# Optimization experiments

Hardware: AMD Instinct MI355X
Metric: run time of the kernel (lower is better)

## Reference

```python
import jax, jax.numpy as jnp
import numpy as np

N_NODES = 100000
N_EDGES = 1_600_000
N_ROIS = 400
HIDDEN = 128
N_GRAPHS = 512
OUT = 2


def setup_inputs() -> dict:
    key = jax.random.key(0)
    ks = jax.random.split(key, 7)
    x = jax.random.normal(ks[0], (N_NODES, N_ROIS), dtype=jnp.float32)
    edge_index = jax.random.randint(ks[1], (2, N_EDGES), 0, N_NODES, dtype=jnp.int32)
    # sorted graph-assignment vector; prepend arange so every graph id is non-empty
    rnd = jax.random.randint(ks[2], (N_NODES - N_GRAPHS,), 0, N_GRAPHS, dtype=jnp.int32)
    batch = jnp.sort(jnp.concatenate([jnp.arange(N_GRAPHS, dtype=jnp.int32), rnd]))
    W = jax.random.normal(ks[3], (N_ROIS, HIDDEN), dtype=jnp.float32) / np.float32(np.sqrt(N_ROIS))
    b = jnp.zeros((HIDDEN,), dtype=jnp.float32)
    lin_W = jax.random.normal(ks[4], (HIDDEN, OUT), dtype=jnp.float32) / np.float32(np.sqrt(HIDDEN))
    lin_b = jnp.zeros((OUT,), dtype=jnp.float32)
    return {"x": x, "edge_index": edge_index, "batch": batch,
            "W": W, "b": b, "lin_W": lin_W, "lin_b": lin_b}


def reference(x, edge_index, batch, W, b, lin_W, lin_b):
    N = x.shape[0]
    # GCNConv: add self-loops, symmetric normalization D^-1/2 (A+I) D^-1/2
    loops = jnp.arange(N, dtype=edge_index.dtype)
    row = jnp.concatenate([edge_index[0], loops])  # source
    col = jnp.concatenate([edge_index[1], loops])  # target
    deg = jax.ops.segment_sum(jnp.ones_like(col, dtype=x.dtype), col, num_segments=N)
    dinv = jnp.where(deg > 0, jax.lax.rsqrt(deg), 0.0)
    norm = dinv[row] * dinv[col]                   # [E+N]
    h = x @ W                                      # [N, H] transform before propagate
    msg = h[row] * norm[:, None]                   # [E+N, H]
    agg = jax.ops.segment_sum(msg, col, num_segments=N) + b
    act = jax.nn.relu(agg)                         # [N, H]
    # global max pool over graph ids (all segments guaranteed non-empty)
    pooled = jax.ops.segment_max(act, batch, num_segments=N_GRAPHS)  # [G, H]
    logits = pooled @ lin_W + lin_b                # [G, OUT]
    return logits, pooled
```

## Files before the change

kernel.cpp:

```cpp
#include <hip/hip_runtime.h>
#include <hip/hip_bf16.h>

#define N_NODES 100000
#define N_EDGES 1600000
#define N_ROIS  400
#define RKP     416
#define HID     128
#define N_GRAPHS 512
#define NOUT    2
#define NBUCK   391
#define BCAP    8192
#define ECH     4096
#define NPW     16

typedef __attribute__((ext_vector_type(8))) short short8;
typedef __attribute__((ext_vector_type(4))) float f32x4;

static __device__ __forceinline__ unsigned short f2bf(float f) {
  unsigned u = __float_as_uint(f);
  u += 0x7fffu + ((u >> 16) & 1u);
  return (unsigned short)(u >> 16);
}
static __device__ __forceinline__ float bf2f(unsigned short h) {
  return __uint_as_float(((unsigned)h) << 16);
}

static __device__ __forceinline__ void gload_lds16(const unsigned short* g, short* l) {
  __builtin_amdgcn_global_load_lds(
      (const __attribute__((address_space(1))) void*)g,
      (__attribute__((address_space(3))) void*)l, 16, 0, 0);
}

__global__ __launch_bounds__(256) void bucket_k(
    const int* __restrict__ row, const int* __restrict__ col,
    int* __restrict__ bcnt, unsigned int* __restrict__ pairs) {
  __shared__ int hist[NBUCK];
  __shared__ int base[NBUCK];
  int t = threadIdx.x;
  for (int b = t; b < NBUCK; b += 256) hist[b] = 0;
  __syncthreads();
  int e0 = blockIdx.x * ECH;
  unsigned int pk[16];
  int bk[16], rk[16];
#pragma unroll
  for (int i = 0; i < 16; ++i) {
    int e = e0 + t + i * 256;
    if (e < N_EDGES) {
      int r = row[e], c = col[e];
      bk[i] = c >> 8;
      pk[i] = ((unsigned)r << 8) | (unsigned)(c & 255);
      rk[i] = atomicAdd(&hist[bk[i]], 1);
    } else bk[i] = -1;
  }
  __syncthreads();
  for (int b = t; b < NBUCK; b += 256)
    base[b] = (hist[b] > 0) ? atomicAdd(&bcnt[b], hist[b]) : 0;
  __syncthreads();
#pragma unroll
  for (int i = 0; i < 16; ++i)
    if (bk[i] >= 0) {
      int p = base[bk[i]] + rk[i];
      if (p < BCAP) pairs[(size_t)bk[i] * BCAP + p] = pk[i];
    }
}

__global__ __launch_bounds__(256) void csr_build_k(
    const unsigned int* __restrict__ pairs, const int* __restrict__ bcnt,
    int* __restrict__ csr_row, int* __restrict__ offs, int* __restrict__ cnt,
    float* __restrict__ dinv) {
  __shared__ unsigned int ep[BCAP];
  __shared__ int h[256];
  __shared__ int sc[256];
  __shared__ int cur[256];
  int b = blockIdx.x;
  int t = threadIdx.x;
  int m = min(bcnt[b], BCAP);
  size_t base = (size_t)b * BCAP;
  for (int j = t; j < m; j += 256) ep[j] = pairs[base + j];
  h[t] = 0;
  __syncthreads();
  for (int j = t; j < m; j += 256) atomicAdd(&h[ep[j] & 255u], 1);
  __syncthreads();
  int myc = h[t];
  int mycp = (myc + 3) & ~3;
  sc[t] = mycp;
  __syncthreads();
  for (int off = 1; off < 256; off <<= 1) {
    int v = (t >= off) ? sc[t - off] : 0;
    __syncthreads();
    sc[t] += v;
    __syncthreads();
  }
  int loff = sc[t] - mycp;
  cur[t] = loff;
  int node = b * 256 + t;
  if (node < N_NODES) {
    cnt[node] = myc;
    offs[node] = (int)base + loff;
    dinv[node] = rsqrtf((float)(myc + 1));
  }
  __syncthreads();
  for (int j = t; j < m; j += 256) {
    unsigned int e = ep[j];
    int pos = atomicAdd(&cur[e & 255u], 1);
    if (pos < BCAP) csr_row[base + pos] = (int)(e >> 8);
  }
}

__global__ void prep_wt_k(const float* __restrict__ W, unsigned short* __restrict__ Wf) {
  int idx = blockIdx.x * blockDim.x + threadIdx.x;
  if (idx >= 13 * 8 * 64 * 8) return;
  int u    = idx & 7;
  int lane = (idx >> 3) & 63;
  int nt   = (idx >> 9) & 7;
  int kk5  = idx >> 12;
  int n = nt * 16 + (lane & 15);
  int k = kk5 * 32 + (lane >> 4) * 8 + u;
  Wf[idx] = (k < N_ROIS) ? f2bf(W[k * HID + n]) : (unsigned short)0;
}

__global__ __launch_bounds__(512, 4) void gemm_k(
    const float* __restrict__ x, const unsigned short* __restrict__ Wf,
    const float* __restrict__ dinv, unsigned short* __restrict__ hp) {
  __shared__ __align__(16) short Bs[28672];
  int t = threadIdx.x;
  int lane = t & 63, wv = t >> 6;
  int mrow = lane & 15, kg = lane >> 4;
  int row0 = blockIdx.x * 128;
  int arow = row0 + wv * 16 + mrow;
  bool rowok = arow < N_NODES;
  const float* xp = x + (size_t)arow * N_ROIS;

  f32x4 acc[8];
#pragma unroll
  for (int i = 0; i < 8; ++i) acc[i] = (f32x4){0.f, 0.f, 0.f, 0.f};

#pragma unroll
  for (int c = 0; c < 7; ++c) {
    int ch = wv * 7 + c;
    gload_lds16(Wf + (size_t)ch * 512 + lane * 8, &Bs[ch * 512]);
  }
  asm volatile("s_waitcnt vmcnt(0)" ::: "memory");
  __syncthreads();

#pragma unroll
  for (int kf = 0; kf < 7; ++kf) {
    int k0 = kf * 32 + kg * 8;
    short8 a8;
    if (rowok && k0 + 8 <= N_ROIS) {
      float4 f0 = *(const float4*)(xp + k0);
      float4 f1 = *(const float4*)(xp + k0 + 4);
      a8[0] = (short)f2bf(f0.x); a8[1] = (short)f2bf(f0.y);
      a8[2] = (short)f2bf(f0.z); a8[3] = (short)f2bf(f0.w);
      a8[4] = (short)f2bf(f1.x); a8[5] = (short)f2bf(f1.y);
      a8[6] = (short)f2bf(f1.z); a8[7] = (short)f2bf(f1.w);
    } else {
#pragma unroll
      for (int u = 0; u < 8; ++u) {
        int k = k0 + u;
        float f = (rowok && k < N_ROIS) ? xp[k] : 0.f;
        a8[u] = (short)f2bf(f);
      }
    }
#pragma unroll
    for (int nt = 0; nt < 8; ++nt) {
      short8 bf = *(const short8*)&Bs[(kf * 8 + nt) * 512 + lane * 8];
      acc[nt] = __builtin_amdgcn_mfma_f32_16x16x32_bf16(a8, bf, acc[nt], 0, 0, 0);
    }
  }
  __syncthreads();

#pragma unroll
  for (int c = 0; c < 6; ++c) {
    int ch = wv * 6 + c;
    gload_lds16(Wf + (size_t)(56 + ch) * 512 + lane * 8, &Bs[ch * 512]);
  }
  asm volatile("s_waitcnt vmcnt(0)" ::: "memory");
  __syncthreads();

#pragma unroll
  for (int kf = 0; kf < 6; ++kf) {
    int k0 = (kf + 7) * 32 + kg * 8;
    short8 a8;
    if (rowok && k0 + 8 <= N_ROIS) {
      float4 f0 = *(const float4*)(xp + k0);
      float4 f1 = *(const float4*)(xp + k0 + 4);
      a8[0] = (short)f2bf(f0.x); a8[1] = (short)f2bf(f0.y);
      a8[2] = (short)f2bf(f0.z); a8[3] = (short)f2bf(f0.w);
      a8[4] = (short)f2bf(f1.x); a8[5] = (short)f2bf(f1.y);
      a8[6] = (short)f2bf(f1.z); a8[7] = (short)f2bf(f1.w);
    } else {
#pragma unroll
      for (int u = 0; u < 8; ++u) {
        int k = k0 + u;
        float f = (rowok && k < N_ROIS) ? xp[k] : 0.f;
        a8[u] = (short)f2bf(f);
      }
    }
#pragma unroll
    for (int nt = 0; nt < 8; ++nt) {
      short8 bf = *(const short8*)&Bs[(kf * 8 + nt) * 512 + lane * 8];
      acc[nt] = __builtin_amdgcn_mfma_f32_16x16x32_bf16(a8, bf, acc[nt], 0, 0, 0);
    }
  }

#pragma unroll
  for (int r = 0; r < 4; ++r) {
    int grow = row0 + wv * 16 + kg * 4 + r;
    if (grow < N_NODES) {
      float di = dinv[grow];
      unsigned short* op = hp + (size_t)grow * HID + mrow;
#pragma unroll
      for (int nt = 0; nt < 8; ++nt) op[nt * 16] = f2bf(di * acc[nt][r]);
    }
  }
}

static __device__ __forceinline__ void acc8(float* a, uint4 u) {
  a[0] += bf2f((unsigned short)(u.x));
  a[1] += bf2f((unsigned short)(u.x >> 16));
  a[2] += bf2f((unsigned short)(u.y));
  a[3] += bf2f((unsigned short)(u.y >> 16));
  a[4] += bf2f((unsigned short)(u.z));
  a[5] += bf2f((unsigned short)(u.z >> 16));
  a[6] += bf2f((unsigned short)(u.w));
  a[7] += bf2f((unsigned short)(u.w >> 16));
}

__global__ __launch_bounds__(256) void gather_k(
    const unsigned short* __restrict__ hp, const int* __restrict__ csr_row,
    const int* __restrict__ offs, const int* __restrict__ cnt,
    const float* __restrict__ dinv, const int* __restrict__ batch,
    const float* __restrict__ bias, unsigned int* __restrict__ pooled_bits) {
  int wave = (blockIdx.x * blockDim.x + threadIdx.x) >> 6;
  int lane = threadIdx.x & 63;
  int g  = lane >> 4;
  int cg = lane & 15;
  int n0 = wave * NPW;
  if (n0 >= N_NODES) return;
  int nend = min(n0 + NPW, N_NODES);
  float bv[8];
  {
    float4 b0 = *(const float4*)(bias + cg * 8);
    float4 b1 = *(const float4*)(bias + cg * 8 + 4);
    bv[0] = b0.x; bv[1] = b0.y; bv[2] = b0.z; bv[3] = b0.w;
    bv[4] = b1.x; bv[5] = b1.y; bv[6] = b1.z; bv[7] = b1.w;
  }
  float rm[8];
#pragma unroll
  for (int k = 0; k < 8; ++k) rm[k] = 0.f;
  int cur_g = batch[n0];

  for (int i = n0; i < nend; ++i) {
    int start = offs[i];
    int m = cnt[i];
    float a[8];
#pragma unroll
    for (int k = 0; k < 8; ++k) a[k] = 0.f;
    if (g == 0) {
      uint4 u = *(const uint4*)(hp + (size_t)i * HID + cg * 8);
      acc8(a, u);
    }
    for (int j = 0; j < m; j += 4) {
      int4 q = *(const int4*)(csr_row + start + j);
      int s = (g == 0) ? q.x : (g == 1) ? q.y : (g == 2) ? q.z : q.w;
      if (j + g < m) {
        uint4 u = *(const uint4*)(hp + (size_t)s * HID + cg * 8);
        acc8(a, u);
      }
    }
#pragma unroll
    for (int k = 0; k < 8; ++k) {
      a[k] += __shfl_xor(a[k], 16);
      a[k] += __shfl_xor(a[k], 32);
    }
    float di = dinv[i];
    int gb = batch[i];
    if (gb != cur_g) {
      if (lane < 16) {
#pragma unroll
        for (int k = 0; k < 8; ++k)
          atomicMax(&pooled_bits[cur_g * HID + cg * 8 + k], __float_as_uint(rm[k]));
      }
#pragma unroll
      for (int k = 0; k < 8; ++k) rm[k] = 0.f;
      cur_g = gb;
    }
#pragma unroll
    for (int k = 0; k < 8; ++k)
      rm[k] = fmaxf(rm[k], fmaxf(fmaf(di, a[k], bv[k]), 0.f));
  }
  if (lane < 16) {
#pragma unroll
    for (int k = 0; k < 8; ++k)
      atomicMax(&pooled_bits[cur_g * HID + cg * 8 + k], __float_as_uint(rm[k]));
  }
}

__global__ void logits_k(const float* __restrict__ pooled, const float* __restrict__ lin_W,
                         const float* __restrict__ lin_b, float* __restrict__ out) {
  int t = blockIdx.x * blockDim.x + threadIdx.x;
  if (t < N_GRAPHS * NOUT) {
    int g = t >> 1, o = t & 1;
    float s = lin_b[o];
    const float* pg = pooled + g * HID;
#pragma unroll 8
    for (int k = 0; k < HID; ++k) s = fmaf(pg[k], lin_W[k * NOUT + o], s);
    out[t] = s;
  }
}

extern "C" void kernel_launch(void* const* d_in, const int* in_sizes, int n_in,
                              void* d_out, int out_size, void* d_ws, size_t ws_size,
                              hipStream_t stream) {
  (void)in_sizes; (void)n_in; (void)ws_size;
  const float* x     = (const float*)d_in[0];
  const int*   ei    = (const int*)d_in[1];
  const int*   row   = ei;
  const int*   col   = ei + N_EDGES;
  const int*   batch = (const int*)d_in[2];
  const float* W     = (const float*)d_in[3];
  const float* b     = (const float*)d_in[4];
  const float* lin_W = (const float*)d_in[5];
  const float* lin_b = (const float*)d_in[6];
  float* out = (float*)d_out;

  char* ws = (char*)d_ws;
  int*   bcnt    = (int*)(ws + 0);
  int*   offs    = (int*)(ws + 4096);
  int*   cnt     = (int*)(ws + 404096);
  float* dinv    = (float*)(ws + 804096);
  unsigned short* Wf = (unsigned short*)(ws + 1204096);
  int*   csr_row = (int*)(ws + 1310720);
  unsigned int* pairs = (unsigned int*)(ws + 14123008);
  unsigned short* hp  = (unsigned short*)(ws + 14123008);

  hipMemsetAsync(bcnt, 0, NBUCK * sizeof(int), stream);
  hipMemsetAsync(d_out, 0, (size_t)out_size * sizeof(float), stream);

  bucket_k<<<(N_EDGES + ECH - 1) / ECH, 256, 0, stream>>>(row, col, bcnt, pairs);
  csr_build_k<<<NBUCK, 256, 0, stream>>>(pairs, bcnt, csr_row, offs, cnt, dinv);
  prep_wt_k<<<(13 * 8 * 64 * 8 + 255) / 256, 256, 0, stream>>>(W, Wf);
  gemm_k<<<(N_NODES + 127) / 128, 512, 0, stream>>>(x, Wf, dinv, hp);
  {
    int waves = (N_NODES + NPW - 1) / NPW;
    int blocks = (waves * 64 + 255) / 256;
    gather_k<<<blocks, 256, 0, stream>>>(
        hp, csr_row, offs, cnt, dinv, batch, b,
        (unsigned int*)(out + N_GRAPHS * NOUT));
  }
  logits_k<<<(N_GRAPHS * NOUT + 255) / 256, 256, 0, stream>>>(
      out + N_GRAPHS * NOUT, lin_W, lin_b, out);
}
```

Baseline: 395.6 us.

## Merge bucket/weight-prep and CSR-build/GEMM launches; move dinv scaling into gather

Weight repacking now runs as extra blocks of the edge-bucketing kernel, and CSR construction runs as extra blocks of the GEMM kernel, which cuts two launches and lets independent work overlap. To remove the GEMM's dependency on dinv, the source-side normalization moves into the gather: each neighbor's dinv is loaded per edge and applied with an FMA. hp gets its own workspace region so it no longer aliases pairs. The cost is an extra scattered 4-byte dinv load per edge in the gather, and CSR blocks now occupy 512-thread blocks with half their threads idle in the scan.

```diff
diff --git a/kernel.cpp b/kernel.cpp
--- a/kernel.cpp
+++ b/kernel.cpp
@@ -4,7 +4,6 @@
 #define N_NODES 100000
 #define N_EDGES 1600000
 #define N_ROIS  400
-#define RKP     416
 #define HID     128
 #define N_GRAPHS 512
 #define NOUT    2
@@ -12,6 +11,9 @@
 #define BCAP    8192
 #define ECH     4096
 #define NPW     16
+#define NBLK_BUCKET 391
+#define NBLK_PREP   208
+#define NBLK_GEMM   782
 
 typedef __attribute__((ext_vector_type(8))) short short8;
 typedef __attribute__((ext_vector_type(4))) float f32x4;
@@ -31,12 +33,26 @@
       (__attribute__((address_space(3))) void*)l, 16, 0, 0);
 }
 
-__global__ __launch_bounds__(256) void bucket_k(
+__global__ __launch_bounds__(256) void prep_bucket_k(
     const int* __restrict__ row, const int* __restrict__ col,
-    int* __restrict__ bcnt, unsigned int* __restrict__ pairs) {
+    int* __restrict__ bcnt, unsigned int* __restrict__ pairs,
+    const float* __restrict__ W, unsigned short* __restrict__ Wf) {
   __shared__ int hist[NBUCK];
   __shared__ int base[NBUCK];
   int t = threadIdx.x;
+  if (blockIdx.x >= NBLK_BUCKET) {
+    int idx = (blockIdx.x - NBLK_BUCKET) * 256 + t;
+    if (idx < 13 * 8 * 64 * 8) {
+      int u    = idx & 7;
+      int lane = (idx >> 3) & 63;
+      int nt   = (idx >> 9) & 7;
+      int kk5  = idx >> 12;
+      int n = nt * 16 + (lane & 15);
+      int k = kk5 * 32 + (lane >> 4) * 8 + u;
+      Wf[idx] = (k < N_ROIS) ? f2bf(W[k * HID + n]) : (unsigned short)0;
+    }
+    return;
+  }
   for (int b = t; b < NBUCK; b += 256) hist[b] = 0;
   __syncthreads();
   int e0 = blockIdx.x * ECH;
@@ -64,69 +80,60 @@
     }
 }
 
-__global__ __launch_bounds__(256) void csr_build_k(
+__global__ __launch_bounds__(512, 4) void csr_gemm_k(
     const unsigned int* __restrict__ pairs, const int* __restrict__ bcnt,
     int* __restrict__ csr_row, int* __restrict__ offs, int* __restrict__ cnt,
-    float* __restrict__ dinv) {
-  __shared__ unsigned int ep[BCAP];
-  __shared__ int h[256];
-  __shared__ int sc[256];
-  __shared__ int cur[256];
-  int b = blockIdx.x;
+    float* __restrict__ dinv,
+    const float* __restrict__ x, const unsigned short* __restrict__ Wf,
+    unsigned short* __restrict__ hp) {
+  __shared__ __align__(16) union {
+    struct { unsigned int ep[BCAP]; int h[256]; int sc[256]; int cur[256]; } c;
+    short Bs[28672];
+  } u;
   int t = threadIdx.x;
-  int m = min(bcnt[b], BCAP);
-  size_t base = (size_t)b * BCAP;
-  for (int j = t; j < m; j += 256) ep[j] = pairs[base + j];
-  h[t] = 0;
-  __syncthreads();
-  for (int j = t; j < m; j += 256) atomicAdd(&h[ep[j] & 255u], 1);
-  __syncthreads();
-  int myc = h[t];
-  int mycp = (myc + 3) & ~3;
-  sc[t] = mycp;
-  __syncthreads();
-  for (int off = 1; off < 256; off <<= 1) {
-    int v = (t >= off) ? sc[t - off] : 0;
+
+  if (blockIdx.x < NBUCK) {
+    bool act = t < 256;
+    int b = blockIdx.x;
+    int m = min(bcnt[b], BCAP);
+    size_t base = (size_t)b * BCAP;
+    for (int j = t; j < m; j += 512) u.c.ep[j] = pairs[base + j];
+    if (act) u.c.h[t] = 0;
     __syncthreads();
-    sc[t] += v;
+    for (int j = t; j < m; j += 512) atomicAdd(&u.c.h[u.c.ep[j] & 255u], 1);
     __syncthreads();
-  }
-  int loff = sc[t] - mycp;
-  cur[t] = loff;
-  int node = b * 256 + t;
-  if (node < N_NODES) {
-    cnt[node] = myc;
-    offs[node] = (int)base + loff;
-    dinv[node] = rsqrtf((float)(myc + 1));
-  }
-  __syncthreads();
-  for (int j = t; j < m; j += 256) {
-    unsigned int e = ep[j];
-    int pos = atomicAdd(&cur[e & 255u], 1);
-    if (pos < BCAP) csr_row[base + pos] = (int)(e >> 8);
-  }
-}
-
-__global__ void prep_wt_k(const float* __restrict__ W, unsigned short* __restrict__ Wf) {
-  int idx = blockIdx.x * blockDim.x + threadIdx.x;
-  if (idx >= 13 * 8 * 64 * 8) return;
-  int u    = idx & 7;
-  int lane = (idx >> 3) & 63;
-  int nt   = (idx >> 9) & 7;
-  int kk5  = idx >> 12;
-  int n = nt * 16 + (lane & 15);
-  int k = kk5 * 32 + (lane >> 4) * 8 + u;
-  Wf[idx] = (k < N_ROIS) ? f2bf(W[k * HID + n]) : (unsigned short)0;
-}
-
-__global__ __launch_bounds__(512, 4) void gemm_k(
-    const float* __restrict__ x, const unsigned short* __restrict__ Wf,
-    const float* __restrict__ dinv, unsigned short* __restrict__ hp) {
-  __shared__ __align__(16) short Bs[28672];
-  int t = threadIdx.x;
+    int myc = act ? u.c.h[t] : 0;
+    int mycp = (myc + 3) & ~3;
+    if (act) u.c.sc[t] = mycp;
+    __syncthreads();
+    for (int off = 1; off < 256; off <<= 1) {
+      int v = (act && t >= off) ? u.c.sc[t - off] : 0;
+      __syncthreads();
+      if (act) u.c.sc[t] += v;
+      __syncthreads();
+    }
+    if (act) {
+      int loff = u.c.sc[t] - mycp;
+      u.c.cur[t] = loff;
+      int node = b * 256 + t;
+      if (node < N_NODES) {
+        cnt[node] = myc;
+        offs[node] = (int)base + loff;
+        dinv[node] = rsqrtf((float)(myc + 1));
+      }
+    }
+    __syncthreads();
+    for (int j = t; j < m; j += 512) {
+      unsigned int e = u.c.ep[j];
+      int pos = atomicAdd(&u.c.cur[e & 255u], 1);
+      if (pos < BCAP) csr_row[base + pos] = (int)(e >> 8);
+    }
+    return;
+  }
+
   int lane = t & 63, wv = t >> 6;
   int mrow = lane & 15, kg = lane >> 4;
-  int row0 = blockIdx.x * 128;
+  int row0 = (blockIdx.x - NBUCK) * 128;
   int arow = row0 + wv * 16 + mrow;
   bool rowok = arow < N_NODES;
   const float* xp = x + (size_t)arow * N_ROIS;
@@ -138,7 +145,7 @@
 #pragma unroll
   for (int c = 0; c < 7; ++c) {
     int ch = wv * 7 + c;
-    gload_lds16(Wf + (size_t)ch * 512 + lane * 8, &Bs[ch * 512]);
+    gload_lds16(Wf + (size_t)ch * 512 + lane * 8, &u.Bs[ch * 512]);
   }
   asm volatile("s_waitcnt vmcnt(0)" ::: "memory");
   __syncthreads();
@@ -156,15 +163,15 @@
       a8[6] = (short)f2bf(f1.z); a8[7] = (short)f2bf(f1.w);
     } else {
 #pragma unroll
-      for (int u = 0; u < 8; ++u) {
-        int k = k0 + u;
+      for (int v = 0; v < 8; ++v) {
+        int k = k0 + v;
         float f = (rowok && k < N_ROIS) ? xp[k] : 0.f;
-        a8[u] = (short)f2bf(f);
+        a8[v] = (short)f2bf(f);
       }
     }
 #pragma unroll
     for (int nt = 0; nt < 8; ++nt) {
-      short8 bf = *(const short8*)&Bs[(kf * 8 + nt) * 512 + lane * 8];
+      short8 bf = *(const short8*)&u.Bs[(kf * 8 + nt) * 512 + lane * 8];
       acc[nt] = __builtin_amdgcn_mfma_f32_16x16x32_bf16(a8, bf, acc[nt], 0, 0, 0);
     }
   }
@@ -173,7 +180,7 @@
 #pragma unroll
   for (int c = 0; c < 6; ++c) {
     int ch = wv * 6 + c;
-    gload_lds16(Wf + (size_t)(56 + ch) * 512 + lane * 8, &Bs[ch * 512]);
+    gload_lds16(Wf + (size_t)(56 + ch) * 512 + lane * 8, &u.Bs[ch * 512]);
   }
   asm volatile("s_waitcnt vmcnt(0)" ::: "memory");
   __syncthreads();
@@ -191,15 +198,15 @@
       a8[6] = (short)f2bf(f1.z); a8[7] = (short)f2bf(f1.w);
     } else {
 #pragma unroll
-      for (int u = 0; u < 8; ++u) {
-        int k = k0 + u;
+      for (int v = 0; v < 8; ++v) {
+        int k = k0 + v;
         float f = (rowok && k < N_ROIS) ? xp[k] : 0.f;
-        a8[u] = (short)f2bf(f);
+        a8[v] = (short)f2bf(f);
       }
     }
 #pragma unroll
     for (int nt = 0; nt < 8; ++nt) {
-      short8 bf = *(const short8*)&Bs[(kf * 8 + nt) * 512 + lane * 8];
+      short8 bf = *(const short8*)&u.Bs[(kf * 8 + nt) * 512 + lane * 8];
       acc[nt] = __builtin_amdgcn_mfma_f32_16x16x32_bf16(a8, bf, acc[nt], 0, 0, 0);
     }
   }
@@ -208,23 +215,22 @@
   for (int r = 0; r < 4; ++r) {
     int grow = row0 + wv * 16 + kg * 4 + r;
     if (grow < N_NODES) {
-      float di = dinv[grow];
       unsigned short* op = hp + (size_t)grow * HID + mrow;
 #pragma unroll
-      for (int nt = 0; nt < 8; ++nt) op[nt * 16] = f2bf(di * acc[nt][r]);
-    }
-  }
-}
-
-static __device__ __forceinline__ void acc8(float* a, uint4 u) {
-  a[0] += bf2f((unsigned short)(u.x));
-  a[1] += bf2f((unsigned short)(u.x >> 16));
-  a[2] += bf2f((unsigned short)(u.y));
-  a[3] += bf2f((unsigned short)(u.y >> 16));
-  a[4] += bf2f((unsigned short)(u.z));
-  a[5] += bf2f((unsigned short)(u.z >> 16));
-  a[6] += bf2f((unsigned short)(u.w));
-  a[7] += bf2f((unsigned short)(u.w >> 16));
+      for (int nt = 0; nt < 8; ++nt) op[nt * 16] = f2bf(acc[nt][r]);
+    }
+  }
+}
+
+static __device__ __forceinline__ void acc8s(float* a, uint4 u, float d) {
+  a[0] = fmaf(d, bf2f((unsigned short)(u.x)), a[0]);
+  a[1] = fmaf(d, bf2f((unsigned short)(u.x >> 16)), a[1]);
+  a[2] = fmaf(d, bf2f((unsigned short)(u.y)), a[2]);
+  a[3] = fmaf(d, bf2f((unsigned short)(u.y >> 16)), a[3]);
+  a[4] = fmaf(d, bf2f((unsigned short)(u.z)), a[4]);
+  a[5] = fmaf(d, bf2f((unsigned short)(u.z >> 16)), a[5]);
+  a[6] = fmaf(d, bf2f((unsigned short)(u.w)), a[6]);
+  a[7] = fmaf(d, bf2f((unsigned short)(u.w >> 16)), a[7]);
 }
 
 __global__ __launch_bounds__(256) void gather_k(
@@ -254,19 +260,21 @@
   for (int i = n0; i < nend; ++i) {
     int start = offs[i];
     int m = cnt[i];
+    float di = dinv[i];
     float a[8];
 #pragma unroll
     for (int k = 0; k < 8; ++k) a[k] = 0.f;
     if (g == 0) {
       uint4 u = *(const uint4*)(hp + (size_t)i * HID + cg * 8);
-      acc8(a, u);
+      acc8s(a, u, di);
     }
     for (int j = 0; j < m; j += 4) {
       int4 q = *(const int4*)(csr_row + start + j);
       int s = (g == 0) ? q.x : (g == 1) ? q.y : (g == 2) ? q.z : q.w;
       if (j + g < m) {
+        float dv = dinv[s];
         uint4 u = *(const uint4*)(hp + (size_t)s * HID + cg * 8);
-        acc8(a, u);
+        acc8s(a, u, dv);
       }
     }
 #pragma unroll
@@ -274,7 +282,6 @@
       a[k] += __shfl_xor(a[k], 16);
       a[k] += __shfl_xor(a[k], 32);
     }
-    float di = dinv[i];
     int gb = batch[i];
     if (gb != cur_g) {
       if (lane < 16) {
@@ -333,15 +340,14 @@
   unsigned short* Wf = (unsigned short*)(ws + 1204096);
   int*   csr_row = (int*)(ws + 1310720);
   unsigned int* pairs = (unsigned int*)(ws + 14123008);
-  unsigned short* hp  = (unsigned short*)(ws + 14123008);
+  unsigned short* hp  = (unsigned short*)(ws + 26935296);
 
   hipMemsetAsync(bcnt, 0, NBUCK * sizeof(int), stream);
   hipMemsetAsync(d_out, 0, (size_t)out_size * sizeof(float), stream);
 
-  bucket_k<<<(N_EDGES + ECH - 1) / ECH, 256, 0, stream>>>(row, col, bcnt, pairs);
-  csr_build_k<<<NBUCK, 256, 0, stream>>>(pairs, bcnt, csr_row, offs, cnt, dinv);
-  prep_wt_k<<<(13 * 8 * 64 * 8 + 255) / 256, 256, 0, stream>>>(W, Wf);
-  gemm_k<<<(N_NODES + 127) / 128, 512, 0, stream>>>(x, Wf, dinv, hp);
+  prep_bucket_k<<<NBLK_BUCKET + NBLK_PREP, 256, 0, stream>>>(row, col, bcnt, pairs, W, Wf);
+  csr_gemm_k<<<NBUCK + NBLK_GEMM, 512, 0, stream>>>(
+      pairs, bcnt, csr_row, offs, cnt, dinv, x, Wf, hp);
   {
     int waves = (N_NODES + NPW - 1) / NPW;
     int blocks = (waves * 64 + 255) / 256;
```

Result: faster. 385.5 us (-2.6%).
